# Performance work log

Measured on AMD Instinct MI355X. Metric: run time of the kernel, lower is better.

## Reference

```python
import jax, jax.numpy as jnp
import numpy as np

B, C, H, W = 32, 1024, 32, 32
KC, VC = 1024, 1024  # key_channels must equal H*W; value_channels must equal in_channels


def setup_inputs() -> dict:
    key = jax.random.key(0)
    ks = jax.random.split(key, 8)
    s = 1.0 / np.sqrt(C)
    return {
        "x": jax.random.normal(ks[0], (B, C, H, W), dtype=jnp.float32),
        "Wq": jax.random.normal(ks[1], (KC, C), dtype=jnp.float32) * s,
        "bq": jax.random.normal(ks[2], (KC,), dtype=jnp.float32) * 0.01,
        "Wk": jax.random.normal(ks[3], (KC, C), dtype=jnp.float32) * s,
        "bk": jax.random.normal(ks[4], (KC,), dtype=jnp.float32) * 0.01,
        "Wv": jax.random.normal(ks[5], (VC, C), dtype=jnp.float32) * s,
        "bv": jax.random.normal(ks[6], (VC,), dtype=jnp.float32) * 0.01,
        # torch init is zeros(1); use a nonzero scalar so the attention path is exercised
        "gamma": jax.random.normal(ks[7], (1,), dtype=jnp.float32) * 0.5,
    }


def reference(x, Wq, bq, Wk, bk, Wv, bv, gamma):
    b, c, h, w = x.shape
    n = h * w
    xf = x.reshape(b, c, n)  # [B, C, N]
    # 1x1 convs == per-position channel projections
    q = jnp.einsum('kc,bcn->bkn', Wq, xf) + bq[None, :, None]  # [B, Kc, N]
    k = jnp.einsum('kc,bcn->bkn', Wk, xf) + bk[None, :, None]  # [B, Kc, N]
    v = jnp.einsum('vc,bcn->bvn', Wv, xf) + bv[None, :, None]  # [B, Cv, N]
    # bmm(query, key^T): contracts spatial dim -> channel-channel attention [B, Kc, Kc]
    attn = jax.nn.softmax(jnp.einsum('bin,bjn->bij', q, k), axis=-1)
    # bmm(value, attention): value's spatial dim (== Kc) contracts with attn rows
    out = jnp.einsum('bvn,bnk->bvk', v, attn)  # [B, Cv, Kc] with Kc == N
    out = out.reshape(b, -1, h, w)
    return gamma * out + x
```

## Files before the change

### kernel.cpp

```cpp
#include <hip/hip_runtime.h>
#include <cstdint>

typedef __fp16 f16x8 __attribute__((ext_vector_type(8)));
typedef __fp16 f16x4 __attribute__((ext_vector_type(4)));
typedef float  f32x4 __attribute__((ext_vector_type(4)));

static constexpr int NDIM = 1024;

static constexpr long long OFF_W     = 0;
static constexpr long long OFF_BIAS  = 6291456;
static constexpr long long OFF_XT    = 6303744;
static constexpr long long OFF_S     = 0;
static constexpr long long OFF_QKV   = 134217728;
static constexpr long long OFF_STATS = OFF_QKV + 2097152;

__device__ __forceinline__ void async16(__fp16* lds, const __fp16* g) {
  __builtin_amdgcn_global_load_lds(
      (const __attribute__((address_space(1))) void*)g,
      (__attribute__((address_space(3))) void*)lds, 16, 0, 0);
}

__global__ __launch_bounds__(256) void cast_w(const float* __restrict__ Wq,
                                              const float* __restrict__ Wk,
                                              const float* __restrict__ Wv,
                                              __fp16* __restrict__ W3) {
  const int i = blockIdx.x * 256 + threadIdx.x;
  const int which = i >> 18;
  const int j = i & 262143;
  const float* src = which == 0 ? Wq : (which == 1 ? Wk : Wv);
  const float4 v = ((const float4*)src)[j];
  f16x4 o = {(__fp16)v.x, (__fp16)v.y, (__fp16)v.z, (__fp16)v.w};
  ((f16x4*)W3)[i] = o;
}

__global__ __launch_bounds__(256) void pack_bias(const float* __restrict__ bq,
                                                 const float* __restrict__ bk,
                                                 const float* __restrict__ bv,
                                                 float* __restrict__ b3) {
  const int i = blockIdx.x * 256 + threadIdx.x;
  if (i < 1024) b3[i] = bq[i];
  else if (i < 2048) b3[i] = bk[i - 1024];
  else if (i < 3072) b3[i] = bv[i - 2048];
}

__global__ __launch_bounds__(256) void transpose_cast_x(const float* __restrict__ x,
                                                        __fp16* __restrict__ xT) {
  __shared__ float t[32][33];
  const int b = blockIdx.z;
  const int n0 = blockIdx.x * 32, c0 = blockIdx.y * 32;
  const float* xb = x + (long long)b * NDIM * NDIM;
  __fp16* ob = xT + (long long)b * NDIM * NDIM;
  const int tx = threadIdx.x & 31, ty = threadIdx.x >> 5;
#pragma unroll
  for (int i = ty; i < 32; i += 8)
    t[i][tx] = xb[(long long)(c0 + i) * NDIM + n0 + tx];
  __syncthreads();
#pragma unroll
  for (int i = ty; i < 32; i += 8)
    ob[(long long)(n0 + i) * NDIM + c0 + tx] = (__fp16)t[tx][i];
}


#define STAGE_A(NXT, h, kk)                                                        \
  async16(&As[(NXT)*16384 + (h)*8192 + 0*4096 + tid*8],                            \
          A + (long long)(m0 + (h)*128 + 0*64 + a_r) * K + (kk) + a_c);            \
  async16(&As[(NXT)*16384 + (h)*8192 + 1*4096 + tid*8],                            \
          A + (long long)(m0 + (h)*128 + 1*64 + a_r) * K + (kk) + a_c);

#define STAGE_B(NXT, s, kk)                                                        \
  async16(&Bs[(NXT)*16384 + (s)*8192 + 0*4096 + tid*8],                            \
          Bp + (long long)(n0 + 0*128 + b_r) * K + (kk) + (s)*32 + b_c);           \
  async16(&Bs[(NXT)*16384 + (s)*8192 + 1*4096 + tid*8],                            \
          Bp + (long long)(n0 + 1*128 + b_r) * K + (kk) + (s)*32 + b_c);

#define LOAD_AF(CUR, ks)                                                           \
  _Pragma("unroll")                                                                \
  for (int mf = 0; mf < 8; ++mf)                                                   \
    af[mf] = *(const f16x8*)&As[(CUR)*16384 + aRow + mf*1024 + acol##ks];

#define LOAD_BF(CUR, ks, nfb)                                                      \
  bf[0] = *(const f16x8*)&Bs[(CUR)*16384 + (ks)*8192 + bRow + (nfb)*512 + bcol];   \
  bf[1] = *(const f16x8*)&Bs[(CUR)*16384 + (ks)*8192 + bRow + ((nfb)+1)*512 + bcol];

#define MFMA16(nfb)                                                                \
  __builtin_amdgcn_s_setprio(1);                                                   \
  _Pragma("unroll")                                                                \
  for (int mf = 0; mf < 8; ++mf) {                                                 \
    acc[mf][nfb]     = __builtin_amdgcn_mfma_f32_16x16x32_f16(af[mf], bf[0], acc[mf][nfb], 0, 0, 0);      \
    acc[mf][(nfb)+1] = __builtin_amdgcn_mfma_f32_16x16x32_f16(af[mf], bf[1], acc[mf][(nfb)+1], 0, 0, 0);  \
  }                                                                                \
  __builtin_amdgcn_s_setprio(0);

#define TILE(CUR, NXT, KNEXT)                                                      \
  asm volatile("s_waitcnt vmcnt(2)" ::: "memory");                                 \
  __builtin_amdgcn_s_barrier();                                                    \
  asm volatile("" ::: "memory");                                                   \
  STAGE_A(NXT, 0, KNEXT)                                                           \
  LOAD_AF(CUR, 0)                                                                  \
  LOAD_BF(CUR, 0, 0)                                                               \
  MFMA16(0)                                                                        \
  STAGE_A(NXT, 1, KNEXT)                                                           \
  LOAD_BF(CUR, 0, 2)                                                               \
  MFMA16(2)                                                                        \
  asm volatile("s_waitcnt vmcnt(4)" ::: "memory");                                 \
  __builtin_amdgcn_s_barrier();                                                    \
  asm volatile("" ::: "memory");                                                   \
  STAGE_B(NXT, 0, KNEXT)                                                           \
  LOAD_AF(CUR, 1)                                                                  \
  LOAD_BF(CUR, 1, 0)                                                               \
  MFMA16(0)                                                                        \
  STAGE_B(NXT, 1, KNEXT)                                                           \
  LOAD_BF(CUR, 1, 2)                                                               \
  MFMA16(2)

template <int EPI>
__global__ __launch_bounds__(512, 2)
void gemm256(const __fp16* __restrict__ Ag, const __fp16* __restrict__ Bg,
             void* __restrict__ Cout, const float* __restrict__ bias,
             const float* __restrict__ X, const float* __restrict__ gamma,
             int M, int N, int K, long long sA, long long sB, long long sC) {
  __shared__ alignas(16) __fp16 As[2 * 16384];
  __shared__ alignas(16) __fp16 Bs[2 * 16384];

  const int tid  = threadIdx.x;
  const int wid  = tid >> 6, lane = tid & 63;
  const int wm   = wid >> 2, wn = wid & 3;
  const int g    = lane >> 4, r = lane & 15;
  const int b    = blockIdx.z;
  const int m0   = blockIdx.y * 256;
  const int n0   = blockIdx.x * 256;

  const __fp16* A  = Ag + (long long)b * sA;
  const __fp16* Bp = Bg + (long long)b * sB;

  const int a_r = tid >> 3;
  const int a_c = ((tid & 7) ^ ((tid >> 3) & 7)) * 8;
  const int b_r = tid >> 2;
  const int b_c = ((tid & 3) ^ ((tid >> 2) & 3)) * 8;

  const int aRow  = (wm * 128 + r) * 64;
  const int acol0 = (((0 * 64) + g * 16) ^ ((r & 7) << 4)) >> 1;
  const int acol1 = (((1 * 64) + g * 16) ^ ((r & 7) << 4)) >> 1;
  const int bRow  = (wn * 64 + r) * 32;
  const int bcol  = ((g * 16) ^ ((r & 3) << 4)) >> 1;

  f16x8 af[8];
  f16x8 bf[2];
  f32x4 acc[8][4];
#pragma unroll
  for (int i = 0; i < 8; ++i)
#pragma unroll
    for (int j = 0; j < 4; ++j) acc[i][j] = f32x4{0.f, 0.f, 0.f, 0.f};

  STAGE_A(0, 0, 0)
  STAGE_A(0, 1, 0)
  STAGE_B(0, 0, 0)
  STAGE_B(0, 1, 0)

  for (int k0 = 0; k0 < K; k0 += 128) {
    const int kn1 = k0 + 64;
    const int kn2 = (k0 + 128 < K) ? (k0 + 128) : 0;
    TILE(0, 1, kn1)
    TILE(1, 0, kn2)
  }

  const float g2 = (EPI == 2) ? gamma[0] : 0.f;
  const int ccol  = n0 + wn * 64 + (lane & 15);
  const int crow0 = m0 + wm * 128 + (lane >> 4) * 4;
#pragma unroll
  for (int mf = 0; mf < 8; ++mf) {
#pragma unroll
    for (int reg = 0; reg < 4; ++reg) {
      const int row = crow0 + mf * 16 + reg;
      const long long rb = (long long)b * sC + (long long)row * N;
      const float bb = (EPI == 0) ? bias[row] : 0.f;
#pragma unroll
      for (int nf = 0; nf < 4; ++nf) {
        const int col = ccol + nf * 16;
        const float v = acc[mf][nf][reg];
        if (EPI == 0)      ((__fp16*)Cout)[rb + col] = (__fp16)(v + bb);
        else if (EPI == 1) ((float*)Cout)[rb + col] = v;
        else               ((float*)Cout)[rb + col] = g2 * v + X[rb + col];
      }
    }
  }
}

__global__ __launch_bounds__(256) void row_stats(const float* __restrict__ S,
                                                 float2* __restrict__ stats) {
  const int row = blockIdx.x * 4 + (threadIdx.x >> 6);
  const int lane = threadIdx.x & 63;
  const float4* rp = (const float4*)(S + (long long)row * NDIM);
  float4 v[4];
  float m = -3.4e38f;
#pragma unroll
  for (int j = 0; j < 4; j++) {
    v[j] = rp[lane + 64 * j];
    m = fmaxf(m, fmaxf(fmaxf(v[j].x, v[j].y), fmaxf(v[j].z, v[j].w)));
  }
#pragma unroll
  for (int o = 32; o; o >>= 1) m = fmaxf(m, __shfl_xor(m, o));
  float s = 0.f;
#pragma unroll
  for (int j = 0; j < 4; j++)
    s += __expf(v[j].x - m) + __expf(v[j].y - m) + __expf(v[j].z - m) + __expf(v[j].w - m);
#pragma unroll
  for (int o = 32; o; o >>= 1) s += __shfl_xor(s, o);
  if (lane == 0) stats[row] = make_float2(m, 1.f / s);
}

__global__ __launch_bounds__(256) void softmax_transpose(const float* __restrict__ S,
                                                         const float2* __restrict__ stats,
                                                         __fp16* __restrict__ attnT) {
  __shared__ __fp16 t[64][72];
  const int b = blockIdx.z;
  const int i0 = blockIdx.y * 64, j0 = blockIdx.x * 64;
  const float* Sb = S + (long long)b * NDIM * NDIM;
  const float2* st = stats + b * NDIM;
  const int tr = threadIdx.x >> 4;
  const int tc = (threadIdx.x & 15) * 4;
#pragma unroll
  for (int it = 0; it < 4; it++) {
    const int i = tr + 16 * it;
    const float4 vv = *(const float4*)&Sb[(long long)(i0 + i) * NDIM + j0 + tc];
    const float2 ms = st[i0 + i];
    t[tc + 0][i] = (__fp16)(__expf(vv.x - ms.x) * ms.y);
    t[tc + 1][i] = (__fp16)(__expf(vv.y - ms.x) * ms.y);
    t[tc + 2][i] = (__fp16)(__expf(vv.z - ms.x) * ms.y);
    t[tc + 3][i] = (__fp16)(__expf(vv.w - ms.x) * ms.y);
  }
  __syncthreads();
  __fp16* Ab = attnT + (long long)b * 3145728;
#pragma unroll
  for (int it = 0; it < 4; it++) {
    const int j = tr + 16 * it;
    f16x4 o = {t[j][tc], t[j][tc + 1], t[j][tc + 2], t[j][tc + 3]};
    *(f16x4*)&Ab[(long long)(j0 + j) * NDIM + i0 + tc] = o;
  }
}

extern "C" void kernel_launch(void* const* d_in, const int* in_sizes, int n_in,
                              void* d_out, int out_size, void* d_ws, size_t ws_size,
                              hipStream_t stream) {
  const float* x     = (const float*)d_in[0];
  const float* Wq    = (const float*)d_in[1];
  const float* bq    = (const float*)d_in[2];
  const float* Wk    = (const float*)d_in[3];
  const float* bk    = (const float*)d_in[4];
  const float* Wv    = (const float*)d_in[5];
  const float* bv    = (const float*)d_in[6];
  const float* gamma = (const float*)d_in[7];
  char* ws = (char*)d_ws;

  __fp16* W3    = (__fp16*)(ws + OFF_W);
  float*  bias3 = (float*)(ws + OFF_BIAS);
  __fp16* xT    = (__fp16*)(ws + OFF_XT);
  float*  S     = (float*)(ws + OFF_S);
  __fp16* QKV   = (__fp16*)(ws + OFF_QKV);
  float2* stats = (float2*)(ws + OFF_STATS);
  float*  out   = (float*)d_out;

  cast_w<<<3072, 256, 0, stream>>>(Wq, Wk, Wv, W3);
  pack_bias<<<12, 256, 0, stream>>>(bq, bk, bv, bias3);
  transpose_cast_x<<<dim3(32, 32, 32), 256, 0, stream>>>(x, xT);

  gemm256<0><<<dim3(4, 12, 32), 512, 0, stream>>>(
      W3, xT, QKV, bias3, nullptr, nullptr,
      3072, 1024, 1024, 0LL, 1048576LL, 3145728LL);

  gemm256<1><<<dim3(4, 4, 32), 512, 0, stream>>>(
      QKV, QKV + 1048576, S, nullptr, nullptr, nullptr,
      1024, 1024, 1024, 3145728LL, 3145728LL, 1048576LL);

  row_stats<<<8192, 256, 0, stream>>>(S, stats);
  softmax_transpose<<<dim3(16, 16, 32), 256, 0, stream>>>(S, stats, QKV);

  gemm256<2><<<dim3(4, 4, 32), 512, 0, stream>>>(
      QKV + 2097152, QKV, out, nullptr, x, gamma,
      1024, 1024, 1024, 3145728LL, 3145728LL, 1048576LL);
}
```

Before: 542.5 us.

## Restructure GEMM mainloop into 4-stage K=32 pipeline with deeper prefetch

Replaces the double-buffered K=64 GEMM main loop with a four-buffer ring of K=32 tiles, prefetching three tiles ahead and waiting with vmcnt(8). It also moves to a new XOR-swizzled shared-memory layout, adds sched_barrier and extra s_barriers to interleave fragment loads with MFMA pairs, and hardcodes M/N/K=1024 strides. The aim is to hide global-load latency better and raise MFMA utilisation. The cost is more barriers per K step, and the shared-memory total is unchanged at 128KB.

```diff
diff --git a/kernel.cpp b/kernel.cpp
--- a/kernel.cpp
+++ b/kernel.cpp
@@ -61,66 +61,50 @@
 }
 
 
-#define STAGE_A(NXT, h, kk)                                                        \
-  async16(&As[(NXT)*16384 + (h)*8192 + 0*4096 + tid*8],                            \
-          A + (long long)(m0 + (h)*128 + 0*64 + a_r) * K + (kk) + a_c);            \
-  async16(&As[(NXT)*16384 + (h)*8192 + 1*4096 + tid*8],                            \
-          A + (long long)(m0 + (h)*128 + 1*64 + a_r) * K + (kk) + a_c);
-
-#define STAGE_B(NXT, s, kk)                                                        \
-  async16(&Bs[(NXT)*16384 + (s)*8192 + 0*4096 + tid*8],                            \
-          Bp + (long long)(n0 + 0*128 + b_r) * K + (kk) + (s)*32 + b_c);           \
-  async16(&Bs[(NXT)*16384 + (s)*8192 + 1*4096 + tid*8],                            \
-          Bp + (long long)(n0 + 1*128 + b_r) * K + (kk) + (s)*32 + b_c);
-
-#define LOAD_AF(CUR, ks)                                                           \
-  _Pragma("unroll")                                                                \
-  for (int mf = 0; mf < 8; ++mf)                                                   \
-    af[mf] = *(const f16x8*)&As[(CUR)*16384 + aRow + mf*1024 + acol##ks];
-
-#define LOAD_BF(CUR, ks, nfb)                                                      \
-  bf[0] = *(const f16x8*)&Bs[(CUR)*16384 + (ks)*8192 + bRow + (nfb)*512 + bcol];   \
-  bf[1] = *(const f16x8*)&Bs[(CUR)*16384 + (ks)*8192 + bRow + ((nfb)+1)*512 + bcol];
-
-#define MFMA16(nfb)                                                                \
-  __builtin_amdgcn_s_setprio(1);                                                   \
-  _Pragma("unroll")                                                                \
-  for (int mf = 0; mf < 8; ++mf) {                                                 \
-    acc[mf][nfb]     = __builtin_amdgcn_mfma_f32_16x16x32_f16(af[mf], bf[0], acc[mf][nfb], 0, 0, 0);      \
-    acc[mf][(nfb)+1] = __builtin_amdgcn_mfma_f32_16x16x32_f16(af[mf], bf[1], acc[mf][(nfb)+1], 0, 0, 0);  \
-  }                                                                                \
-  __builtin_amdgcn_s_setprio(0);
-
-#define TILE(CUR, NXT, KNEXT)                                                      \
-  asm volatile("s_waitcnt vmcnt(2)" ::: "memory");                                 \
-  __builtin_amdgcn_s_barrier();                                                    \
-  asm volatile("" ::: "memory");                                                   \
-  STAGE_A(NXT, 0, KNEXT)                                                           \
-  LOAD_AF(CUR, 0)                                                                  \
-  LOAD_BF(CUR, 0, 0)                                                               \
-  MFMA16(0)                                                                        \
-  STAGE_A(NXT, 1, KNEXT)                                                           \
-  LOAD_BF(CUR, 0, 2)                                                               \
-  MFMA16(2)                                                                        \
-  asm volatile("s_waitcnt vmcnt(4)" ::: "memory");                                 \
-  __builtin_amdgcn_s_barrier();                                                    \
-  asm volatile("" ::: "memory");                                                   \
-  STAGE_B(NXT, 0, KNEXT)                                                           \
-  LOAD_AF(CUR, 1)                                                                  \
-  LOAD_BF(CUR, 1, 0)                                                               \
-  MFMA16(0)                                                                        \
-  STAGE_B(NXT, 1, KNEXT)                                                           \
-  LOAD_BF(CUR, 1, 2)                                                               \
-  MFMA16(2)
+#define STAGE_A(NXT, KN)                                                            \
+  async16(&As[(NXT)*8192 + tid*8],        A  + (long long)(m0 + sRow)       * 1024 + (KN) + sCol); \
+  async16(&As[(NXT)*8192 + 4096 + tid*8], A  + (long long)(m0 + 128 + sRow) * 1024 + (KN) + sCol);
+
+#define STAGE_B(NXT, KN)                                                            \
+  async16(&Bs[(NXT)*8192 + tid*8],        Bp + (long long)(n0 + sRow)       * 1024 + (KN) + sCol); \
+  async16(&Bs[(NXT)*8192 + 4096 + tid*8], Bp + (long long)(n0 + 128 + sRow) * 1024 + (KN) + sCol);
+
+#define MFMA_PAIR(NF)                                                               \
+  __builtin_amdgcn_s_setprio(1);                                                    \
+  _Pragma("unroll")                                                                 \
+  for (int mf = 0; mf < 8; ++mf) {                                                  \
+    acc[mf][NF]     = __builtin_amdgcn_mfma_f32_16x16x32_f16(af[mf], bf[NF],     acc[mf][NF], 0, 0, 0);     \
+    acc[mf][NF + 1] = __builtin_amdgcn_mfma_f32_16x16x32_f16(af[mf], bf[NF + 1], acc[mf][NF + 1], 0, 0, 0); \
+  }                                                                                 \
+  __builtin_amdgcn_s_setprio(0);                                                    \
+  __builtin_amdgcn_sched_barrier(0);
+
+#define TILE(BUF, NXT, KN)                                                          \
+  asm volatile("s_waitcnt vmcnt(8)" ::: "memory");                                  \
+  __builtin_amdgcn_s_barrier();                                                     \
+  STAGE_A(NXT, KN)                                                                  \
+  _Pragma("unroll")                                                                 \
+  for (int mf = 0; mf < 8; ++mf)                                                    \
+    af[mf] = *(const f16x8*)&As[(BUF)*8192 + aBase + mf*512];                       \
+  bf[0] = *(const f16x8*)&Bs[(BUF)*8192 + bBase + 0*512];                           \
+  bf[1] = *(const f16x8*)&Bs[(BUF)*8192 + bBase + 1*512];                           \
+  __builtin_amdgcn_s_barrier();                                                     \
+  MFMA_PAIR(0)                                                                      \
+  __builtin_amdgcn_s_barrier();                                                     \
+  STAGE_B(NXT, KN)                                                                  \
+  bf[2] = *(const f16x8*)&Bs[(BUF)*8192 + bBase + 2*512];                           \
+  bf[3] = *(const f16x8*)&Bs[(BUF)*8192 + bBase + 3*512];                           \
+  __builtin_amdgcn_s_barrier();                                                     \
+  MFMA_PAIR(2)
 
 template <int EPI>
 __global__ __launch_bounds__(512, 2)
 void gemm256(const __fp16* __restrict__ Ag, const __fp16* __restrict__ Bg,
              void* __restrict__ Cout, const float* __restrict__ bias,
              const float* __restrict__ X, const float* __restrict__ gamma,
-             int M, int N, int K, long long sA, long long sB, long long sC) {
-  __shared__ alignas(16) __fp16 As[2 * 16384];
-  __shared__ alignas(16) __fp16 Bs[2 * 16384];
+             long long sA, long long sB, long long sC) {
+  __shared__ alignas(16) __fp16 As[4 * 8192];
+  __shared__ alignas(16) __fp16 Bs[4 * 8192];
 
   const int tid  = threadIdx.x;
   const int wid  = tid >> 6, lane = tid & 63;
@@ -133,35 +117,35 @@
   const __fp16* A  = Ag + (long long)b * sA;
   const __fp16* Bp = Bg + (long long)b * sB;
 
-  const int a_r = tid >> 3;
-  const int a_c = ((tid & 7) ^ ((tid >> 3) & 7)) * 8;
-  const int b_r = tid >> 2;
-  const int b_c = ((tid & 3) ^ ((tid >> 2) & 3)) * 8;
-
-  const int aRow  = (wm * 128 + r) * 64;
-  const int acol0 = (((0 * 64) + g * 16) ^ ((r & 7) << 4)) >> 1;
-  const int acol1 = (((1 * 64) + g * 16) ^ ((r & 7) << 4)) >> 1;
-  const int bRow  = (wn * 64 + r) * 32;
-  const int bcol  = ((g * 16) ^ ((r & 3) << 4)) >> 1;
+  const int sRow = tid >> 2;
+  const int sCol = ((tid & 3) ^ ((tid >> 3) & 3)) * 8;
+
+  const int fcol  = (g ^ ((r >> 1) & 3)) * 8;
+  const int aBase = (wm * 128 + r) * 32 + fcol;
+  const int bBase = (wn * 64 + r) * 32 + fcol;
 
   f16x8 af[8];
-  f16x8 bf[2];
+  f16x8 bf[4];
   f32x4 acc[8][4];
 #pragma unroll
   for (int i = 0; i < 8; ++i)
 #pragma unroll
     for (int j = 0; j < 4; ++j) acc[i][j] = f32x4{0.f, 0.f, 0.f, 0.f};
 
-  STAGE_A(0, 0, 0)
-  STAGE_A(0, 1, 0)
-  STAGE_B(0, 0, 0)
-  STAGE_B(0, 1, 0)
-
-  for (int k0 = 0; k0 < K; k0 += 128) {
-    const int kn1 = k0 + 64;
-    const int kn2 = (k0 + 128 < K) ? (k0 + 128) : 0;
-    TILE(0, 1, kn1)
-    TILE(1, 0, kn2)
+  STAGE_A(0, 0)  STAGE_B(0, 0)
+  STAGE_A(1, 32) STAGE_B(1, 32)
+  STAGE_A(2, 64) STAGE_B(2, 64)
+
+  for (int t0 = 0; t0 < 1024; t0 += 128) {
+    const int ka  = t0 + 96;
+    const int k0n = (ka < 1024) ? ka : 0;
+    const int k1n = (ka + 32 < 1024) ? ka + 32 : 0;
+    const int k2n = (ka + 64 < 1024) ? ka + 64 : 0;
+    const int k3n = (ka + 96 < 1024) ? ka + 96 : 0;
+    TILE(0, 3, k0n)
+    TILE(1, 0, k1n)
+    TILE(2, 1, k2n)
+    TILE(3, 2, k3n)
   }
 
   const float g2 = (EPI == 2) ? gamma[0] : 0.f;
@@ -172,7 +156,7 @@
 #pragma unroll
     for (int reg = 0; reg < 4; ++reg) {
       const int row = crow0 + mf * 16 + reg;
-      const long long rb = (long long)b * sC + (long long)row * N;
+      const long long rb = (long long)b * sC + (long long)row * 1024;
       const float bb = (EPI == 0) ? bias[row] : 0.f;
 #pragma unroll
       for (int nf = 0; nf < 4; ++nf) {
@@ -266,16 +250,16 @@
 
   gemm256<0><<<dim3(4, 12, 32), 512, 0, stream>>>(
       W3, xT, QKV, bias3, nullptr, nullptr,
-      3072, 1024, 1024, 0LL, 1048576LL, 3145728LL);
+      0LL, 1048576LL, 3145728LL);
 
   gemm256<1><<<dim3(4, 4, 32), 512, 0, stream>>>(
       QKV, QKV + 1048576, S, nullptr, nullptr, nullptr,
-      1024, 1024, 1024, 3145728LL, 3145728LL, 1048576LL);
+      3145728LL, 3145728LL, 1048576LL);
 
   row_stats<<<8192, 256, 0, stream>>>(S, stats);
   softmax_transpose<<<dim3(16, 16, 32), 256, 0, stream>>>(S, stats, QKV);
 
   gemm256<2><<<dim3(4, 4, 32), 512, 0, stream>>>(
       QKV + 2097152, QKV, out, nullptr, x, gamma,
-      1024, 1024, 1024, 3145728LL, 3145728LL, 1048576LL);
-}
+      3145728LL, 3145728LL, 1048576LL);
+}
```

After: 555.5 us. 1.02x slower.
